# Performance work log

Hardware: AMD Instinct MI355X
Metric: run time of the kernel (lower is better)

## Reference

```python
import jax, jax.numpy as jnp
import numpy as np

B, S, E, H = 4, 2048, 1024, 16
D = E // H  # key_size


def setup_inputs() -> dict:
    key = jax.random.key(0)
    ks = jax.random.split(key, 6)
    s = 1.0 / np.sqrt(E)
    return {
        "X": jax.random.normal(ks[0], (B, S, E), dtype=jnp.float32),
        "Wq": jax.random.uniform(ks[1], (E, E), jnp.float32, -s, s),
        "Wk": jax.random.uniform(ks[2], (E, E), jnp.float32, -s, s),
        "Wv": jax.random.uniform(ks[3], (E, E), jnp.float32, -s, s),
        "Wo": jax.random.uniform(ks[4], (E, E), jnp.float32, -s, s),
        "bo": jax.random.uniform(ks[5], (E,), jnp.float32, -s, s),
    }


def reference(X, Wq, Wk, Wv, Wo, bo):
    # Linear layers: y = x @ W^T (torch convention), no bias for q/k/v
    def split(x):  # [B,S,E] -> [B,H,S,D]
        return x.reshape(B, S, H, D).transpose(0, 2, 1, 3)

    q = split(X @ Wq.T)
    k = split(X @ Wk.T)
    v = split(X @ Wv.T)
    scale = jnp.asarray(np.sqrt(D), dtype=X.dtype)
    scores = jnp.einsum("bhqd,bhkd->bhqk", q, k) / scale
    probs = jax.nn.softmax(scores, axis=-1)
    ctx = jnp.einsum("bhqk,bhkd->bhqd", probs, v)
    out = ctx.transpose(0, 2, 1, 3).reshape(B, S, E)
    return out @ Wo.T + bo
```

## Files before the change

kernel.cpp:

```cpp
#include <hip/hip_runtime.h>
#include <hip/hip_bf16.h>

typedef short bf16x8 __attribute__((ext_vector_type(8)));
typedef float f32x4  __attribute__((ext_vector_type(4)));

__device__ __forceinline__ short f2bf(float f) {
    union { float f; unsigned u; } x; x.f = f;
    unsigned r = x.u + 0x7fffu + ((x.u >> 16) & 1u);
    return (short)(r >> 16);
}

__device__ __forceinline__ unsigned rbits(float f) {
    union { float f; unsigned u; } x; x.f = f;
    return x.u + 0x8000u;
}
__device__ __forceinline__ int pack2(float a, float b) {
    return (int)__builtin_amdgcn_perm(rbits(b), rbits(a), 0x07060302u);
}

__device__ __forceinline__ f32x4 mfma32k(bf16x8 a, bf16x8 b, f32x4 c) {
    return __builtin_amdgcn_mfma_f32_16x16x32_bf16(a, b, c, 0, 0, 0);
}

#define GLDS16(g, l)                                                            \
    __builtin_amdgcn_global_load_lds(                                           \
        (const __attribute__((address_space(1))) void*)(g),                     \
        (__attribute__((address_space(3))) void*)(l), 16, 0, 0)

static constexpr int Bb = 4, Ss = 2048, Ee = 1024, Hh = 16, Dd = 64;
static constexpr int Mrows = Bb * Ss;
static constexpr float CL2 = 0.1803368801111204f;

__global__ void cvt_all(const float* __restrict__ X,  const float* __restrict__ Wq,
                        const float* __restrict__ Wk, const float* __restrict__ Wv,
                        const float* __restrict__ Wo,
                        short* __restrict__ Xb, short* __restrict__ Wqk,
                        short* __restrict__ Wvb, short* __restrict__ Wob) {
    int bid = blockIdx.x;
    const float* src; short* dst; int off; float scale = 1.0f;
    if (bid < 8192) {
        src = X; dst = Xb; off = bid * 1024;
    } else {
        int wsel = (bid - 8192) >> 10;
        off = ((bid - 8192) & 1023) * 1024;
        if      (wsel == 0) { src = Wq; dst = Wqk;                scale = CL2; }
        else if (wsel == 1) { src = Wk; dst = Wqk + Ee * Ee; }
        else if (wsel == 2) { src = Wv; dst = Wvb; }
        else                { src = Wo; dst = Wob; }
    }
    int i = off + threadIdx.x * 4;
    float4 v = *(const float4*)(src + i);
    short4 o;
    o.x = f2bf(v.x * scale); o.y = f2bf(v.y * scale);
    o.z = f2bf(v.z * scale); o.w = f2bf(v.w * scale);
    *(short4*)(dst + i) = o;
}

__device__ __forceinline__ void gemm_pipe_256x128(
    short* lds, const short* hA, const short* hB,
    int wv, int lane16, int fsw0, int fsw1,
    f32x4 (&acc)[4][4])
{
#define STG(gsrc, matOff, half, j, T, buf)                                      \
    GLDS16((gsrc) + ((half) * 128 + (j) * 64) * 1024 + (T) * 64,                \
           lds + (buf) * 32768 + (matOff) + (half) * 8192 + (j) * 4096 + wv * 512)

    STG(hA, 0,     0, 0, 0, 0); STG(hA, 0,     0, 1, 0, 0);
    STG(hA, 0,     1, 0, 0, 0); STG(hA, 0,     1, 1, 0, 0);
    STG(hB, 16384, 0, 0, 0, 0); STG(hB, 16384, 0, 1, 0, 0);
    STG(hA, 0,     0, 0, 1, 1); STG(hA, 0,     0, 1, 1, 1);
    asm volatile("s_waitcnt vmcnt(2)" ::: "memory");
    __builtin_amdgcn_s_barrier();

    const int wm2 = wv & 3, wn2 = wv >> 2;
    const int aoff = (wm2 * 64 + lane16) * 64;
    const int boff = (wn2 * 64 + lane16) * 64;

    for (int T = 0; T < 16; ++T) {
        const int cur = T & 1, nxt = cur ^ 1;
        const short* sAc = lds + cur * 32768;
        const short* sBc = sAc + 16384;
        bf16x8 bb[4][2];
#pragma unroll
        for (int nj = 0; nj < 4; ++nj) {
            bb[nj][0] = *(const bf16x8*)(sBc + boff + nj * 1024 + fsw0);
            bb[nj][1] = *(const bf16x8*)(sBc + boff + nj * 1024 + fsw1);
        }
        bf16x8 a0, a1, a2, a3;
        a0 = *(const bf16x8*)(sAc + aoff + 0 * 1024 + fsw0);
        a1 = *(const bf16x8*)(sAc + aoff + 0 * 1024 + fsw1);
        a2 = *(const bf16x8*)(sAc + aoff + 1 * 1024 + fsw0);
        a3 = *(const bf16x8*)(sAc + aoff + 1 * 1024 + fsw1);
        if (T < 15) {
            STG(hA, 0,     1, 0, T + 1, nxt); STG(hA, 0,     1, 1, T + 1, nxt);
            STG(hB, 16384, 0, 0, T + 1, nxt); STG(hB, 16384, 0, 1, T + 1, nxt);
        }
        __builtin_amdgcn_s_barrier();
        __builtin_amdgcn_s_setprio(1);
#pragma unroll
        for (int nj = 0; nj < 4; ++nj) {
            acc[0][nj] = mfma32k(a0, bb[nj][0], acc[0][nj]);
            acc[0][nj] = mfma32k(a1, bb[nj][1], acc[0][nj]);
            acc[1][nj] = mfma32k(a2, bb[nj][0], acc[1][nj]);
            acc[1][nj] = mfma32k(a3, bb[nj][1], acc[1][nj]);
        }
        __builtin_amdgcn_s_setprio(0);
        __builtin_amdgcn_s_barrier();
        a0 = *(const bf16x8*)(sAc + aoff + 2 * 1024 + fsw0);
        a1 = *(const bf16x8*)(sAc + aoff + 2 * 1024 + fsw1);
        a2 = *(const bf16x8*)(sAc + aoff + 3 * 1024 + fsw0);
        a3 = *(const bf16x8*)(sAc + aoff + 3 * 1024 + fsw1);
        __builtin_amdgcn_s_barrier();
        __builtin_amdgcn_s_setprio(1);
#pragma unroll
        for (int nj = 0; nj < 4; ++nj) {
            acc[2][nj] = mfma32k(a0, bb[nj][0], acc[2][nj]);
            acc[2][nj] = mfma32k(a1, bb[nj][1], acc[2][nj]);
            acc[3][nj] = mfma32k(a2, bb[nj][0], acc[3][nj]);
            acc[3][nj] = mfma32k(a3, bb[nj][1], acc[3][nj]);
        }
        __builtin_amdgcn_s_setprio(0);
        __builtin_amdgcn_s_barrier();
        if (T < 14) {
            STG(hA, 0, 0, 0, T + 2, cur); STG(hA, 0, 0, 1, T + 2, cur);
            asm volatile("s_waitcnt vmcnt(2)" ::: "memory");
            __builtin_amdgcn_s_barrier();
        } else if (T == 14) {
            asm volatile("s_waitcnt vmcnt(0)" ::: "memory");
            __builtin_amdgcn_s_barrier();
        }
    }
#undef STG
}

__global__ __launch_bounds__(512, 2)
void gemm_fused(const short* __restrict__ A0, const short* __restrict__ B0,
                short* __restrict__ C0,
                const short* __restrict__ A1, const short* __restrict__ B1,
                short* __restrict__ C1) {
    __shared__ __align__(16) short lds[65536];
    const int t = threadIdx.x, l = t & 63, wv = t >> 6;
    const int lane16 = l & 15, quad = l >> 4;
    const int wm = wv >> 2, wn = wv & 3;

    int bid = blockIdx.x;
    const int xcd = bid & 7, ib = bid >> 3;
    const int bm = xcd * 4 + (ib & 3), bn = ib >> 2;

    const int grow = t >> 3;
    const int lsl  = ((t & 7) ^ ((t >> 3) & 7)) * 8;
    const short* gA = A0 + (size_t)(bm * 256 + grow) * 1024 + lsl;
    const short* gB = B0 + (size_t)(bn * 256 + grow) * 1024 + lsl;

#define STAGE8(gsrc, matOff, half, j, T, buf)                                   \
    GLDS16((gsrc) + ((half) * 128 + (j) * 64) * 1024 + (T) * 64,                \
           lds + (buf) * 32768 + (matOff) + (half) * 8192 + (j) * 4096 + wv * 512)

    const int fsw0 = ((quad)     ^ (lane16 & 7)) * 8;
    const int fsw1 = ((quad + 4) ^ (lane16 & 7)) * 8;
    const int aoff = (wm * 128 + lane16) * 64;
    const int boff = (wn * 64  + lane16) * 64;

    f32x4 acc[8][4] = {};

    STAGE8(gA, 0,     0, 0, 0, 0); STAGE8(gA, 0,     0, 1, 0, 0);
    STAGE8(gA, 0,     1, 0, 0, 0); STAGE8(gA, 0,     1, 1, 0, 0);
    STAGE8(gB, 16384, 0, 0, 0, 0); STAGE8(gB, 16384, 0, 1, 0, 0);
    STAGE8(gB, 16384, 1, 0, 0, 0); STAGE8(gB, 16384, 1, 1, 0, 0);
    STAGE8(gA, 0,     0, 0, 1, 1); STAGE8(gA, 0,     0, 1, 1, 1);
    asm volatile("s_waitcnt vmcnt(2)" ::: "memory");
    __builtin_amdgcn_s_barrier();

#define ARD(MI0)                                                                \
    a0 = *(const bf16x8*)(sAc + aoff + (MI0) * 1024 + fsw0);                    \
    a1 = *(const bf16x8*)(sAc + aoff + (MI0) * 1024 + fsw1);                    \
    a2 = *(const bf16x8*)(sAc + aoff + ((MI0) + 1) * 1024 + fsw0);              \
    a3 = *(const bf16x8*)(sAc + aoff + ((MI0) + 1) * 1024 + fsw1);

#define MFQ(MI0)                                                                \
    __builtin_amdgcn_s_setprio(1);                                              \
    _Pragma("unroll")                                                           \
    for (int nj = 0; nj < 4; ++nj) {                                            \
        acc[MI0][nj]       = mfma32k(a0, bf[nj][0], acc[MI0][nj]);              \
        acc[MI0][nj]       = mfma32k(a1, bf[nj][1], acc[MI0][nj]);              \
        acc[(MI0) + 1][nj] = mfma32k(a2, bf[nj][0], acc[(MI0) + 1][nj]);        \
        acc[(MI0) + 1][nj] = mfma32k(a3, bf[nj][1], acc[(MI0) + 1][nj]);        \
    }                                                                           \
    __builtin_amdgcn_s_setprio(0);

    for (int T = 0; T < 16; ++T) {
        const int cur = T & 1, nxt = cur ^ 1;
        const short* sAc = lds + cur * 32768;
        const short* sBc = sAc + 16384;
        bf16x8 bf[4][2];
#pragma unroll
        for (int nj = 0; nj < 4; ++nj) {
            bf[nj][0] = *(const bf16x8*)(sBc + boff + nj * 1024 + fsw0);
            bf[nj][1] = *(const bf16x8*)(sBc + boff + nj * 1024 + fsw1);
        }
        bf16x8 a0, a1, a2, a3;
        ARD(0)
        if (T < 15) { STAGE8(gA, 0, 1, 0, T + 1, nxt); STAGE8(gA, 0, 1, 1, T + 1, nxt); }
        __builtin_amdgcn_s_barrier();
        MFQ(0)
        __builtin_amdgcn_s_barrier();
        ARD(2)
        if (T < 15) { STAGE8(gB, 16384, 0, 0, T + 1, nxt); STAGE8(gB, 16384, 0, 1, T + 1, nxt); }
        __builtin_amdgcn_s_barrier();
        MFQ(2)
        __builtin_amdgcn_s_barrier();
        ARD(4)
        if (T < 15) { STAGE8(gB, 16384, 1, 0, T + 1, nxt); STAGE8(gB, 16384, 1, 1, T + 1, nxt); }
        __builtin_amdgcn_s_barrier();
        MFQ(4)
        __builtin_amdgcn_s_barrier();
        ARD(6)
        __builtin_amdgcn_s_barrier();
        MFQ(6)
        __builtin_amdgcn_s_barrier();
        if (T < 14) {
            STAGE8(gA, 0, 0, 0, T + 2, cur); STAGE8(gA, 0, 0, 1, T + 2, cur);
            asm volatile("s_waitcnt vmcnt(2)" ::: "memory");
            __builtin_amdgcn_s_barrier();
        } else if (T == 14) {
            asm volatile("s_waitcnt vmcnt(0)" ::: "memory");
            __builtin_amdgcn_s_barrier();
        }
    }
#undef ARD
#undef MFQ
#undef STAGE8

#pragma unroll
    for (int mi = 0; mi < 8; ++mi)
#pragma unroll
        for (int nj = 0; nj < 4; ++nj) {
            int row = bm * 256 + wm * 128 + mi * 16 + quad * 4;
            int col = bn * 256 + wn * 64 + nj * 16 + lane16;
#pragma unroll
            for (int r = 0; r < 4; ++r)
                C0[(size_t)(row + r) * 2048 + col] = f2bf(acc[mi][nj][r]);
        }

    const int vbm = ib >> 3, vbn = xcd * 8 + (ib & 7);
    const short* hA = A1 + (size_t)(vbm * 256 + grow) * 1024 + lsl;
    const short* hB = B1 + (size_t)(vbn * 128 + grow) * 1024 + lsl;
    f32x4 accB[4][4] = {};
    gemm_pipe_256x128(lds, hA, hB, wv, lane16, fsw0, fsw1, accB);

    const int wm2 = wv & 3, wn2 = wv >> 2;
    const int sEven = (lane16 >> 2) * 8 + (lane16 & 3);
#pragma unroll
    for (int mi = 0; mi < 4; ++mi)
#pragma unroll
        for (int nj = 0; nj < 4; ++nj) {
            int row = vbm * 256 + wm2 * 64 + mi * 16 + quad * 4;
            int col = vbn * 128 + wn2 * 64 + nj * 16 + lane16;
            col = (col & ~31) | (sEven + (nj & 1) * 4);
#pragma unroll
            for (int r = 0; r < 4; ++r)
                C1[(size_t)(row + r) * 8192 + col] = f2bf(accB[mi][nj][r]);
        }
}

__global__ __launch_bounds__(512, 2)
void gemm_out(const short* __restrict__ A, const short* __restrict__ Bm,
              float* __restrict__ C, const float* __restrict__ bias) {
    __shared__ __align__(16) short lds[65536];
    const int t = threadIdx.x, l = t & 63, wv = t >> 6;
    const int lane16 = l & 15, quad = l >> 4;

    int bid = blockIdx.x;
    const int xcd = bid & 7, ib = bid >> 3;
    const int bm = xcd * 4 + (ib & 3), bn = ib >> 2;

    const int grow = t >> 3;
    const int lsl  = ((t & 7) ^ ((t >> 3) & 7)) * 8;
    const short* hA = A  + (size_t)(bm * 256 + grow) * 1024 + lsl;
    const short* hB = Bm + (size_t)(bn * 128 + grow) * 1024 + lsl;

    const int fsw0 = ((quad)     ^ (lane16 & 7)) * 8;
    const int fsw1 = ((quad + 4) ^ (lane16 & 7)) * 8;

    f32x4 acc[4][4] = {};
    gemm_pipe_256x128(lds, hA, hB, wv, lane16, fsw0, fsw1, acc);

    const int wm2 = wv & 3, wn2 = wv >> 2;
#pragma unroll
    for (int mi = 0; mi < 4; ++mi)
#pragma unroll
        for (int nj = 0; nj < 4; ++nj) {
            int row = bm * 256 + wm2 * 64 + mi * 16 + quad * 4;
            int col = bn * 128 + wn2 * 64 + nj * 16 + lane16;
            float bv = bias[col];
#pragma unroll
            for (int r = 0; r < 4; ++r)
                C[(size_t)(row + r) * 1024 + col] = acc[mi][nj][r] + bv;
        }
}

__global__ __launch_bounds__(256, 4)
void attn_kernel(const short* __restrict__ QK, const short* __restrict__ VT,
                 short* __restrict__ CTX) {
    __shared__ __align__(16) short sK[8192];
    __shared__ __align__(16) short sV[8192];
    const int t = threadIdx.x, w = t >> 6, l = t & 63;
    const int lane16 = l & 15, quad = l >> 4;
    const int bh = blockIdx.x, qt = blockIdx.y;
    const int b = bh >> 4, h = bh & 15;

    const int qx8 = (quad ^ ((lane16 >> 1) & 3)) * 8;

    const short* Qb = QK + ((size_t)(b * 2048 + qt * 128)) * 2048 + h * 64;
    const short* Vb = VT + ((size_t)(h * 64)) * 8192 + (size_t)b * 2048;
    const int ldsOff = (w * 64) * 8;

    int off_kq[4], off_v[4];
#pragma unroll
    for (int p = 0; p < 4; ++p) {
        int c = p * 256 + t;
        int sw = ((c & 3) ^ ((c >> 3) & 3)) * 8;
        off_kq[p] = ((c >> 2) & 127) * 2048 + (c >> 9) * 32 + sw;
        off_v[p]  = ((c >> 2) & 63) * 8192 + (c >> 8) * 32 + sw;
    }

#pragma unroll
    for (int p = 0; p < 4; ++p)
        GLDS16(Qb + off_kq[p], sK + p * 2048 + ldsOff);
    __syncthreads();
    bf16x8 qf[2][2];
#pragma unroll
    for (int mt = 0; mt < 2; ++mt)
#pragma unroll
        for (int ks = 0; ks < 2; ++ks)
            qf[mt][ks] = *(const bf16x8*)(sK + ks * 4096 + (w * 32 + mt * 16 + lane16) * 32 + qx8);
    __syncthreads();

    const short one = (short)0x3F80;
    const bf16x8 ONE8 = {one, one, one, one, one, one, one, one};
    f32x4 lacc[2] = {};
    f32x4 o[2][4] = {};

    const short* kptr = QK + ((size_t)(b * 2048)) * 2048 + 1024 + h * 64;
    const short* vptr = Vb;

    auto QKB = [&](int a, f32x4 (&sc)[2][2]) {
        __builtin_amdgcn_s_setprio(1);
#pragma unroll
        for (int sub = 0; sub < 2; ++sub) {
            int nt = a * 2 + sub;
            bf16x8 kf0 = *(const bf16x8*)(sK + (nt * 16 + lane16) * 32 + qx8);
            bf16x8 kf1 = *(const bf16x8*)(sK + 4096 + (nt * 16 + lane16) * 32 + qx8);
#pragma unroll
            for (int mt = 0; mt < 2; ++mt) {
                f32x4 z = {};
                z = mfma32k(kf0, qf[mt][0], z);
                z = mfma32k(kf1, qf[mt][1], z);
                sc[mt][sub] = z;
            }
        }
        __builtin_amdgcn_s_setprio(0);
    };
    auto PVB = [&](int a, f32x4 (&sc)[2][2]) {
        bf16x8 pf[2];
#pragma unroll
        for (int mt = 0; mt < 2; ++mt) {
            union { int i[4]; bf16x8 v; } u;
#pragma unroll
            for (int sub = 0; sub < 2; ++sub) {
                f32x4 e;
#pragma unroll
                for (int r = 0; r < 4; ++r)
                    e[r] = __builtin_amdgcn_exp2f(sc[mt][sub][r]);
                u.i[sub * 2]     = pack2(e[0], e[1]);
                u.i[sub * 2 + 1] = pack2(e[2], e[3]);
            }
            pf[mt] = u.v;
        }
        __builtin_amdgcn_s_setprio(1);
#pragma unroll
        for (int mt = 0; mt < 2; ++mt)
            lacc[mt] = mfma32k(pf[mt], ONE8, lacc[mt]);
#pragma unroll
        for (int dt = 0; dt < 4; ++dt) {
            bf16x8 vf = *(const bf16x8*)(sV + a * 2048 + (dt * 16 + lane16) * 32 + qx8);
#pragma unroll
            for (int mt = 0; mt < 2; ++mt)
                o[mt][dt] = mfma32k(pf[mt], vf, o[mt][dt]);
        }
        __builtin_amdgcn_s_setprio(0);
    };

    for (int kt = 0; kt < 16; ++kt) {
#pragma unroll
        for (int p = 0; p < 4; ++p)
            GLDS16(kptr + off_kq[p], sK + p * 2048 + ldsOff);
#pragma unroll
        for (int p = 0; p < 4; ++p)
            GLDS16(vptr + off_v[p], sV + p * 2048 + ldsOff);
        kptr += (size_t)128 * 2048;
        vptr += 128;
        __syncthreads();

        f32x4 scA[2][2], scB[2][2];
        QKB(0, scA);
        QKB(1, scB);  PVB(0, scA);
        QKB(2, scA);  PVB(1, scB);
        QKB(3, scB);  PVB(2, scA);
                      PVB(3, scB);
        __syncthreads();
    }

#pragma unroll
    for (int mt = 0; mt < 2; ++mt)
#pragma unroll
        for (int r = 0; r < 4; ++r) {
            float inv = 1.0f / lacc[mt][r];
            int row = b * 2048 + qt * 128 + w * 32 + mt * 16 + quad * 4 + r;
#pragma unroll
            for (int dt = 0; dt < 4; ++dt)
                CTX[(size_t)row * 1024 + h * 64 + dt * 16 + lane16] = f2bf(o[mt][dt][r] * inv);
        }
}

extern "C" void kernel_launch(void* const* d_in, const int* in_sizes, int n_in,
                              void* d_out, int out_size, void* d_ws, size_t ws_size,
                              hipStream_t stream) {
    const float* X  = (const float*)d_in[0];
    const float* Wq = (const float*)d_in[1];
    const float* Wk = (const float*)d_in[2];
    const float* Wv = (const float*)d_in[3];
    const float* Wo = (const float*)d_in[4];
    const float* bo = (const float*)d_in[5];
    float* out = (float*)d_out;

    char* ws = (char*)d_ws;
    constexpr size_t OFF_XB  = 0;
    constexpr size_t OFF_WQK = OFF_XB  + (size_t)Mrows * Ee * 2;
    constexpr size_t OFF_WV  = OFF_WQK + (size_t)2 * Ee * Ee * 2;
    constexpr size_t OFF_WO  = OFF_WV  + (size_t)Ee * Ee * 2;
    constexpr size_t OFF_QK  = OFF_WO  + (size_t)Ee * Ee * 2;
    constexpr size_t OFF_VT  = OFF_QK  + (size_t)Mrows * 2048 * 2;
    constexpr size_t OFF_CTX = OFF_VT  + (size_t)Ee * Mrows * 2;
    short* Xb   = (short*)(ws + OFF_XB);
    short* Wqk  = (short*)(ws + OFF_WQK);
    short* Wvb  = (short*)(ws + OFF_WV);
    short* Wob  = (short*)(ws + OFF_WO);
    short* QKb  = (short*)(ws + OFF_QK);
    short* VTb  = (short*)(ws + OFF_VT);
    short* CTX  = (short*)(ws + OFF_CTX);

    cvt_all<<<12288, 256, 0, stream>>>(X, Wq, Wk, Wv, Wo, Xb, Wqk, Wvb, Wob);

    gemm_fused<<<256, 512, 0, stream>>>(Xb, Wqk, QKb, Wvb, Xb, VTb);

    attn_kernel<<<dim3(Bb * Hh, Ss / 128), 256, 0, stream>>>(QKb, VTb, CTX);

    gemm_out<<<256, 512, 0, stream>>>(CTX, Wob, out, bo);
}
```

Baseline: 237.9 us.

## Prefetch whole K-tiles two steps ahead and drop intra-iteration barriers

Both fused GEMM phases now issue the entire A/B K-tile load for step T+2 into the just-consumed buffer at the end of each iteration, instead of spreading the T+1 loads across sub-phases. This removes the many barriers that separated LDS reads, staging and MFMA batches within an iteration, leaving one barrier per step plus a vmcnt wait. The aim is to cut synchronisation overhead and let waves run MFMAs without lockstep, at the cost of burstier global loads and less interleaving of memory traffic with compute.

```diff
diff --git a/kernel.cpp b/kernel.cpp
--- a/kernel.cpp
+++ b/kernel.cpp
@@ -56,6 +56,7 @@
     *(short4*)(dst + i) = o;
 }
 
+
 __device__ __forceinline__ void gemm_pipe_256x128(
     short* lds, const short* hA, const short* hB,
     int wv, int lane16, int fsw0, int fsw1,
@@ -64,12 +65,14 @@
 #define STG(gsrc, matOff, half, j, T, buf)                                      \
     GLDS16((gsrc) + ((half) * 128 + (j) * 64) * 1024 + (T) * 64,                \
            lds + (buf) * 32768 + (matOff) + (half) * 8192 + (j) * 4096 + wv * 512)
-
-    STG(hA, 0,     0, 0, 0, 0); STG(hA, 0,     0, 1, 0, 0);
-    STG(hA, 0,     1, 0, 0, 0); STG(hA, 0,     1, 1, 0, 0);
-    STG(hB, 16384, 0, 0, 0, 0); STG(hB, 16384, 0, 1, 0, 0);
-    STG(hA, 0,     0, 0, 1, 1); STG(hA, 0,     0, 1, 1, 1);
-    asm volatile("s_waitcnt vmcnt(2)" ::: "memory");
+#define STAGE_T6(T, buf)                                                        \
+    STG(hA, 0,     0, 0, T, buf); STG(hA, 0,     0, 1, T, buf);                 \
+    STG(hA, 0,     1, 0, T, buf); STG(hA, 0,     1, 1, T, buf);                 \
+    STG(hB, 16384, 0, 0, T, buf); STG(hB, 16384, 0, 1, T, buf);
+
+    STAGE_T6(0, 0)
+    STAGE_T6(1, 1)
+    asm volatile("s_waitcnt vmcnt(6)" ::: "memory");
     __builtin_amdgcn_s_barrier();
 
     const int wm2 = wv & 3, wn2 = wv >> 2;
@@ -77,7 +80,7 @@
     const int boff = (wn2 * 64 + lane16) * 64;
 
     for (int T = 0; T < 16; ++T) {
-        const int cur = T & 1, nxt = cur ^ 1;
+        const int cur = T & 1;
         const short* sAc = lds + cur * 32768;
         const short* sBc = sAc + 16384;
         bf16x8 bb[4][2];
@@ -91,11 +94,6 @@
         a1 = *(const bf16x8*)(sAc + aoff + 0 * 1024 + fsw1);
         a2 = *(const bf16x8*)(sAc + aoff + 1 * 1024 + fsw0);
         a3 = *(const bf16x8*)(sAc + aoff + 1 * 1024 + fsw1);
-        if (T < 15) {
-            STG(hA, 0,     1, 0, T + 1, nxt); STG(hA, 0,     1, 1, T + 1, nxt);
-            STG(hB, 16384, 0, 0, T + 1, nxt); STG(hB, 16384, 0, 1, T + 1, nxt);
-        }
-        __builtin_amdgcn_s_barrier();
         __builtin_amdgcn_s_setprio(1);
 #pragma unroll
         for (int nj = 0; nj < 4; ++nj) {
@@ -105,12 +103,10 @@
             acc[1][nj] = mfma32k(a3, bb[nj][1], acc[1][nj]);
         }
         __builtin_amdgcn_s_setprio(0);
-        __builtin_amdgcn_s_barrier();
         a0 = *(const bf16x8*)(sAc + aoff + 2 * 1024 + fsw0);
         a1 = *(const bf16x8*)(sAc + aoff + 2 * 1024 + fsw1);
         a2 = *(const bf16x8*)(sAc + aoff + 3 * 1024 + fsw0);
         a3 = *(const bf16x8*)(sAc + aoff + 3 * 1024 + fsw1);
-        __builtin_amdgcn_s_barrier();
         __builtin_amdgcn_s_setprio(1);
 #pragma unroll
         for (int nj = 0; nj < 4; ++nj) {
@@ -122,14 +118,14 @@
         __builtin_amdgcn_s_setprio(0);
         __builtin_amdgcn_s_barrier();
         if (T < 14) {
-            STG(hA, 0, 0, 0, T + 2, cur); STG(hA, 0, 0, 1, T + 2, cur);
-            asm volatile("s_waitcnt vmcnt(2)" ::: "memory");
-            __builtin_amdgcn_s_barrier();
+            STAGE_T6(T + 2, cur)
+            asm volatile("s_waitcnt vmcnt(6)" ::: "memory");
         } else if (T == 14) {
             asm volatile("s_waitcnt vmcnt(0)" ::: "memory");
-            __builtin_amdgcn_s_barrier();
-        }
+        }
+        __builtin_amdgcn_s_barrier();
     }
+#undef STAGE_T6
 #undef STG
 }
 
@@ -155,6 +151,11 @@
 #define STAGE8(gsrc, matOff, half, j, T, buf)                                   \
     GLDS16((gsrc) + ((half) * 128 + (j) * 64) * 1024 + (T) * 64,                \
            lds + (buf) * 32768 + (matOff) + (half) * 8192 + (j) * 4096 + wv * 512)
+#define STAGE_TILE_A(T, buf)                                                    \
+    STAGE8(gA, 0,     0, 0, T, buf); STAGE8(gA, 0,     0, 1, T, buf);           \
+    STAGE8(gA, 0,     1, 0, T, buf); STAGE8(gA, 0,     1, 1, T, buf);           \
+    STAGE8(gB, 16384, 0, 0, T, buf); STAGE8(gB, 16384, 0, 1, T, buf);           \
+    STAGE8(gB, 16384, 1, 0, T, buf); STAGE8(gB, 16384, 1, 1, T, buf);
 
     const int fsw0 = ((quad)     ^ (lane16 & 7)) * 8;
     const int fsw1 = ((quad + 4) ^ (lane16 & 7)) * 8;
@@ -163,12 +164,9 @@
 
     f32x4 acc[8][4] = {};
 
-    STAGE8(gA, 0,     0, 0, 0, 0); STAGE8(gA, 0,     0, 1, 0, 0);
-    STAGE8(gA, 0,     1, 0, 0, 0); STAGE8(gA, 0,     1, 1, 0, 0);
-    STAGE8(gB, 16384, 0, 0, 0, 0); STAGE8(gB, 16384, 0, 1, 0, 0);
-    STAGE8(gB, 16384, 1, 0, 0, 0); STAGE8(gB, 16384, 1, 1, 0, 0);
-    STAGE8(gA, 0,     0, 0, 1, 1); STAGE8(gA, 0,     0, 1, 1, 1);
-    asm volatile("s_waitcnt vmcnt(2)" ::: "memory");
+    STAGE_TILE_A(0, 0)
+    STAGE_TILE_A(1, 1)
+    asm volatile("s_waitcnt vmcnt(8)" ::: "memory");
     __builtin_amdgcn_s_barrier();
 
 #define ARD(MI0)                                                                \
@@ -189,7 +187,7 @@
     __builtin_amdgcn_s_setprio(0);
 
     for (int T = 0; T < 16; ++T) {
-        const int cur = T & 1, nxt = cur ^ 1;
+        const int cur = T & 1;
         const short* sAc = lds + cur * 32768;
         const short* sBc = sAc + 16384;
         bf16x8 bf[4][2];
@@ -199,36 +197,22 @@
             bf[nj][1] = *(const bf16x8*)(sBc + boff + nj * 1024 + fsw1);
         }
         bf16x8 a0, a1, a2, a3;
-        ARD(0)
-        if (T < 15) { STAGE8(gA, 0, 1, 0, T + 1, nxt); STAGE8(gA, 0, 1, 1, T + 1, nxt); }
-        __builtin_amdgcn_s_barrier();
-        MFQ(0)
-        __builtin_amdgcn_s_barrier();
-        ARD(2)
-        if (T < 15) { STAGE8(gB, 16384, 0, 0, T + 1, nxt); STAGE8(gB, 16384, 0, 1, T + 1, nxt); }
-        __builtin_amdgcn_s_barrier();
-        MFQ(2)
-        __builtin_amdgcn_s_barrier();
-        ARD(4)
-        if (T < 15) { STAGE8(gB, 16384, 1, 0, T + 1, nxt); STAGE8(gB, 16384, 1, 1, T + 1, nxt); }
-        __builtin_amdgcn_s_barrier();
-        MFQ(4)
-        __builtin_amdgcn_s_barrier();
-        ARD(6)
-        __builtin_amdgcn_s_barrier();
-        MFQ(6)
+        ARD(0) MFQ(0)
+        ARD(2) MFQ(2)
+        ARD(4) MFQ(4)
+        ARD(6) MFQ(6)
         __builtin_amdgcn_s_barrier();
         if (T < 14) {
-            STAGE8(gA, 0, 0, 0, T + 2, cur); STAGE8(gA, 0, 0, 1, T + 2, cur);
-            asm volatile("s_waitcnt vmcnt(2)" ::: "memory");
-            __builtin_amdgcn_s_barrier();
+            STAGE_TILE_A(T + 2, cur)
+            asm volatile("s_waitcnt vmcnt(8)" ::: "memory");
         } else if (T == 14) {
             asm volatile("s_waitcnt vmcnt(0)" ::: "memory");
-            __builtin_amdgcn_s_barrier();
-        }
+        }
+        __builtin_amdgcn_s_barrier();
     }
 #undef ARD
 #undef MFQ
+#undef STAGE_TILE_A
 #undef STAGE8
 
 #pragma unroll
```

Result: slower. 244.2 us (+2.7%).
